# Optimization experiments

Measured on AMD Instinct MI355X. Metric: run time of the kernel, lower is better.

The kernel has to match this reference:

```python
import jax, jax.numpy as jnp
import numpy as np

NUM_HEADS = 16
DIM = 1024


def setup_inputs() -> dict:
    key = jax.random.key(0)
    k1, k2, k3, k4 = jax.random.split(key, 4)
    B, N, C = 4, 2048, DIM
    x = jax.random.normal(k1, (B, N, C), dtype=jnp.float32)
    # weights stored in apply orientation: y = x @ W (+ b)
    W_qkv = jax.random.normal(k2, (C, 3 * C), dtype=jnp.float32) * (C ** -0.5)
    W_out = jax.random.normal(k3, (C, C), dtype=jnp.float32) * (C ** -0.5)
    b_out = jax.random.normal(k4, (C,), dtype=jnp.float32) * 0.01
    return {"hidden_states": x, "W_qkv": W_qkv, "W_out": W_out, "b_out": b_out}


def reference(hidden_states, W_qkv, W_out, b_out):
    B, N, C = hidden_states.shape
    H = NUM_HEADS
    Dh = C // H
    scale = Dh ** -0.5
    qkv = hidden_states @ W_qkv                      # [B, N, 3C]
    qkv = qkv.reshape(B, N, 3, H, Dh).transpose(2, 0, 3, 1, 4)  # [3, B, H, N, Dh]
    q, k, v = qkv[0], qkv[1], qkv[2]
    scores = jnp.einsum('bhnd,bhmd->bhnm', q, k) * scale  # [B, H, N, N]
    probs = jax.nn.softmax(scores, axis=-1)
    out = jnp.einsum('bhnm,bhmd->bhnd', probs, v)    # [B, H, N, Dh]
    out = out.transpose(0, 2, 1, 3).reshape(B, N, C)  # merge heads
    return out @ W_out + b_out                        # dropout p=0 -> identity
```

## Files before the change

### kernel.cpp

```cpp
#include <hip/hip_runtime.h>
#include <hip/hip_bf16.h>
#include <stdint.h>

#define BATCH 4
#define SEQN  2048
#define DIMC  1024
#define NHEADS 16
#define DHEAD 64
#define BH_TOT 64
#define MROWS 8192

typedef __attribute__((ext_vector_type(8))) short bf16x8;
typedef __attribute__((ext_vector_type(4))) float f32x4;

__device__ __forceinline__ unsigned short bf16_rtne(float f){
  union { float f; unsigned u; } v; v.f = f;
  unsigned u = v.u;
  return (unsigned short)((u + 0x7FFFu + ((u >> 16) & 1u)) >> 16);
}
__device__ __forceinline__ float bf16f(unsigned short h){
  union { unsigned u; float f; } v; v.u = ((unsigned)h) << 16;
  return v.f;
}

__device__ __forceinline__ void async16(void* lds, const void* g){
  __builtin_amdgcn_global_load_lds((const __attribute__((address_space(1))) void*)g,
                                   (__attribute__((address_space(3))) void*)lds, 16, 0, 0);
}

__global__ __launch_bounds__(256) void split_rows_k(const float* __restrict__ X,
    unsigned short* __restrict__ O, int nrows, int Kc){
  int q4 = Kc >> 2;
  int total = nrows * q4;
  int idx = blockIdx.x*256 + threadIdx.x;
  if (idx >= total) return;
  int row = idx / q4, c = idx - row*q4;
  const float4 v = *(const float4*)(X + ((size_t)row*Kc + c*4));
  float fv[4] = {v.x, v.y, v.z, v.w};
  unsigned short hi[4], lo[4];
#pragma unroll
  for (int j=0;j<4;j++){ hi[j] = bf16_rtne(fv[j]); lo[j] = bf16_rtne(fv[j] - bf16f(hi[j])); }
  size_t ob = (size_t)row*(2*Kc) + c*4;
  ushort4 h; h.x=hi[0]; h.y=hi[1]; h.z=hi[2]; h.w=hi[3];
  ushort4 l2; l2.x=lo[0]; l2.y=lo[1]; l2.z=lo[2]; l2.w=lo[3];
  *(ushort4*)(O + ob) = h;
  *(ushort4*)(O + ob + Kc) = l2;
}

__global__ __launch_bounds__(256) void transpose_split_k(const float* __restrict__ W,
    unsigned short* __restrict__ Wt, int K, int Nc){
  __shared__ float tile[32][33];
  int tx = threadIdx.x & 31, ty = threadIdx.x >> 5;
  int n0 = blockIdx.x*32, k0 = blockIdx.y*32;
#pragma unroll
  for (int i=0;i<4;i++){
    int k = k0 + ty + i*8;
    tile[ty + i*8][tx] = W[(size_t)k*Nc + n0 + tx];
  }
  __syncthreads();
#pragma unroll
  for (int i=0;i<4;i++){
    int n = n0 + ty + i*8;
    float f = tile[tx][ty + i*8];
    unsigned short hi = bf16_rtne(f);
    unsigned short lo = bf16_rtne(f - bf16f(hi));
    Wt[(size_t)n*(2*K) + k0 + tx] = hi;
    Wt[(size_t)n*(2*K) + K + k0 + tx] = lo;
  }
}

__global__ __launch_bounds__(256) void gemm_split_k(
    const unsigned short* __restrict__ A, const unsigned short* __restrict__ Bt,
    float* __restrict__ C, const float* __restrict__ bias, int M, int Nc, int K)
{
  __shared__ unsigned short a_lds[2][4096];
  __shared__ unsigned short b_lds[2][4096];
  const int t = threadIdx.x, w = t>>6, l = t&63, lg = l>>4, ll = l&15;
  const int wr = w>>1, wc = w&1;
  const int m0 = blockIdx.x*128, n0 = blockIdx.y*128;
  const int ldk = 2*K;
  const int nkt = (3*K) >> 5;
  f32x4 acc[4][4];
#pragma unroll
  for (int m=0;m<4;m++)
#pragma unroll
    for (int n=0;n<4;n++) acc[m][n] = (f32x4){0.f,0.f,0.f,0.f};

  auto stage = [&](int buf, int kt){
    int kp = kt*32;
    int ac = (kp < K)   ? kp : kp - K;
    int bc = (kp < 2*K) ? kp : kp - 2*K;
#pragma unroll
    for (int i=0;i<2;i++){
      int s = t + i*256; int row = s>>2; int sl = s&3; int sl2 = sl ^ (row&3);
      async16(&a_lds[buf][s*8], A + (size_t)(m0+row)*ldk + ac + sl2*8);
    }
#pragma unroll
    for (int i=0;i<2;i++){
      int s = t + i*256; int row = s>>2; int sl = s&3; int sl2 = sl ^ (row&3);
      async16(&b_lds[buf][s*8], Bt + (size_t)(n0+row)*ldk + bc + sl2*8);
    }
  };

  stage(0, 0);
  __syncthreads();
  for (int kt=0; kt<nkt; ++kt){
    int cur = kt&1;
    if (kt+1 < nkt) stage(cur^1, kt+1);
    bf16x8 af[4], bfr[4];
#pragma unroll
    for (int m=0;m<4;m++){
      int row = wr*64 + m*16 + ll;
      af[m] = *(const bf16x8*)&a_lds[cur][row*32 + ((lg ^ (row&3))*8)];
    }
#pragma unroll
    for (int n=0;n<4;n++){
      int row = wc*64 + n*16 + ll;
      bfr[n] = *(const bf16x8*)&b_lds[cur][row*32 + ((lg ^ (row&3))*8)];
    }
#pragma unroll
    for (int m=0;m<4;m++)
#pragma unroll
      for (int n=0;n<4;n++)
        acc[m][n] = __builtin_amdgcn_mfma_f32_16x16x32_bf16(af[m], bfr[n], acc[m][n], 0,0,0);
    __syncthreads();
  }
#pragma unroll
  for (int m=0;m<4;m++)
#pragma unroll
    for (int n=0;n<4;n++){
      int col = n0 + wc*64 + n*16 + ll;
      float bv = bias ? bias[col] : 0.f;
#pragma unroll
      for (int r=0;r<4;r++){
        int row = m0 + wr*64 + m*16 + lg*4 + r;
        C[(size_t)row*Nc + col] = acc[m][n][r] + bv;
      }
    }
}

__global__ __launch_bounds__(256) void split_qk_k(const float* __restrict__ qkv,
    unsigned short* __restrict__ Qo, unsigned short* __restrict__ Ko){
  int idx = blockIdx.x*256 + threadIdx.x;
  int d4 = idx & 15, n = (idx>>4) & (SEQN-1), bh = idx >> 15;
  int b = bh>>4, h = bh&15;
  size_t base = ((size_t)(b*SEQN + n))*3072 + h*64 + d4*4;
  float4 q = *(const float4*)(qkv + base);
  float4 k = *(const float4*)(qkv + base + 1024);
  float fq[4] = {q.x,q.y,q.z,q.w}, fk[4] = {k.x,k.y,k.z,k.w};
  unsigned short qh[4],ql[4],kh[4],kl[4];
#pragma unroll
  for (int j=0;j<4;j++){
    qh[j] = bf16_rtne(fq[j]); ql[j] = bf16_rtne(fq[j] - bf16f(qh[j]));
    kh[j] = bf16_rtne(fk[j]); kl[j] = bf16_rtne(fk[j] - bf16f(kh[j]));
  }
  size_t ob = ((size_t)bh*SEQN + n)*128 + d4*4;
  ushort4 u;
  u.x=qh[0];u.y=qh[1];u.z=qh[2];u.w=qh[3]; *(ushort4*)(Qo+ob) = u;
  u.x=ql[0];u.y=ql[1];u.z=ql[2];u.w=ql[3]; *(ushort4*)(Qo+ob+64) = u;
  u.x=kh[0];u.y=kh[1];u.z=kh[2];u.w=kh[3]; *(ushort4*)(Ko+ob) = u;
  u.x=kl[0];u.y=kl[1];u.z=kl[2];u.w=kl[3]; *(ushort4*)(Ko+ob+64) = u;
}

__global__ __launch_bounds__(256) void build_vt_k(const float* __restrict__ qkv,
    unsigned short* __restrict__ Vt){
  __shared__ float tile[64][65];
  const int mt = blockIdx.x, bh = blockIdx.y;
  const int b = bh>>4, h = bh&15;
  const int t = threadIdx.x;
  const int r = t>>2, seg = t&3;
  size_t src = ((size_t)(b*SEQN + mt*64 + r))*3072 + 2048 + h*64 + seg*16;
#pragma unroll
  for (int j=0;j<4;j++){
    float4 v = *(const float4*)(qkv + src + j*4);
    tile[r][seg*16 + j*4 + 0] = v.x;
    tile[r][seg*16 + j*4 + 1] = v.y;
    tile[r][seg*16 + j*4 + 2] = v.z;
    tile[r][seg*16 + j*4 + 3] = v.w;
  }
  __syncthreads();
  const int d = r, ms = seg;
  unsigned short o16[16];
#pragma unroll
  for (int j=0;j<16;j++) o16[j] = bf16_rtne(tile[ms*16 + j][d]);
  size_t dst = ((size_t)(bh*64 + d))*SEQN + mt*64 + ms*16;
  uint4 u0, u1;
  unsigned* pu = (unsigned*)&u0;
  unsigned* pv = (unsigned*)&u1;
#pragma unroll
  for (int j=0;j<4;j++){
    pu[j] = (unsigned)o16[2*j]   | ((unsigned)o16[2*j+1]<<16);
    pv[j] = (unsigned)o16[8+2*j] | ((unsigned)o16[9+2*j]<<16);
  }
  *(uint4*)(Vt + dst) = u0;
  *(uint4*)(Vt + dst + 8) = u1;
}

__global__ __launch_bounds__(256) void attn_k(const unsigned short* __restrict__ Q,
    const unsigned short* __restrict__ Kh, const unsigned short* __restrict__ Vt,
    float* __restrict__ att)
{
  __shared__ unsigned short k_lds[2][8192];
  __shared__ unsigned short v_lds[2][4096];
  __shared__ unsigned short p_lds[4][1024];
  const int qt = blockIdx.x, bh = blockIdx.y;
  const int b = bh>>4, h = bh&15;
  const int t = threadIdx.x, w = t>>6, l = t&63, lg = l>>4, ll = l&15;
  const size_t kvbase = (size_t)bh*SEQN;

  bf16x8 qf[4];
  {
    size_t qrow = (kvbase + qt*64 + w*16 + ll) * 128;
#pragma unroll
    for (int i=0;i<4;i++)
      qf[i] = *(const bf16x8*)(Q + qrow + i*32 + lg*8);
  }
  f32x4 o[4];
#pragma unroll
  for (int d=0; d<4; d++) o[d] = (f32x4){0.f,0.f,0.f,0.f};
  float lpart[4] = {0.f,0.f,0.f,0.f};

  auto stage = [&](int buf, int kv){
    int m0 = kv*64;
#pragma unroll
    for (int i=0;i<4;i++){
      int s = t + i*256; int row = s>>4; int sl = s&15; int sl2 = sl ^ (row&7);
      async16(&k_lds[buf][s*8], Kh + (kvbase + m0 + row)*128 + sl2*8);
    }
#pragma unroll
    for (int i=0;i<2;i++){
      int s = t + i*256; int row = s>>3; int sl = s&7; int sl2 = sl ^ (row&7);
      async16(&v_lds[buf][s*8], Vt + ((size_t)bh*64 + row)*SEQN + m0 + sl2*8);
    }
  };

  stage(0, 0);
  __syncthreads();
  const int NKV = SEQN/64;
  for (int kv=0; kv<NKV; ++kv){
    int cur = kv&1;
    if (kv+1 < NKV) stage(cur^1, kv+1);
#pragma unroll
    for (int nt=0; nt<4; ++nt){
      bf16x8 kf[4];
      int row = nt*16 + ll;
#pragma unroll
      for (int c=0;c<4;c++){
        int slot = c*4 + lg;
        kf[c] = *(const bf16x8*)&k_lds[cur][row*128 + ((slot ^ (row&7))*8)];
      }
      f32x4 a = (f32x4){0.f,0.f,0.f,0.f};
      a = __builtin_amdgcn_mfma_f32_16x16x32_bf16(qf[0], kf[0], a, 0,0,0);
      a = __builtin_amdgcn_mfma_f32_16x16x32_bf16(qf[1], kf[1], a, 0,0,0);
      a = __builtin_amdgcn_mfma_f32_16x16x32_bf16(qf[0], kf[2], a, 0,0,0);
      a = __builtin_amdgcn_mfma_f32_16x16x32_bf16(qf[1], kf[3], a, 0,0,0);
      a = __builtin_amdgcn_mfma_f32_16x16x32_bf16(qf[2], kf[0], a, 0,0,0);
      a = __builtin_amdgcn_mfma_f32_16x16x32_bf16(qf[3], kf[1], a, 0,0,0);
#pragma unroll
      for (int r=0;r<4;r++){
        float e = __expf(a[r] * 0.125f);
        lpart[r] += e;
        int q = lg*4 + r;
        int col = nt*16 + ll;
        int slot = col >> 3;
        p_lds[w][q*64 + ((slot ^ (q&7))*8) + (col&7)] = bf16_rtne(e);
      }
    }
#pragma unroll
    for (int ks=0; ks<2; ++ks){
      int slot = ks*4 + lg;
      bf16x8 pf = *(const bf16x8*)&p_lds[w][ll*64 + ((slot ^ (ll&7))*8)];
#pragma unroll
      for (int dt=0; dt<4; ++dt){
        int row = dt*16 + ll;
        bf16x8 vf = *(const bf16x8*)&v_lds[cur][row*64 + ((slot ^ (row&7))*8)];
        o[dt] = __builtin_amdgcn_mfma_f32_16x16x32_bf16(pf, vf, o[dt], 0,0,0);
      }
    }
    __syncthreads();
  }
#pragma unroll
  for (int r=0;r<4;r++){
    float s = lpart[r];
    s += __shfl_xor(s, 1);
    s += __shfl_xor(s, 2);
    s += __shfl_xor(s, 4);
    s += __shfl_xor(s, 8);
    float rl = 1.0f / s;
    int qrow = qt*64 + w*16 + lg*4 + r;
    size_t ob = ((size_t)(b*SEQN + qrow))*DIMC + h*64;
#pragma unroll
    for (int dt=0; dt<4; ++dt)
      att[ob + dt*16 + ll] = o[dt][r] * rl;
  }
}

extern "C" void kernel_launch(void* const* d_in, const int* in_sizes, int n_in,
                              void* d_out, int out_size, void* d_ws, size_t ws_size,
                              hipStream_t stream){
  const float* x    = (const float*)d_in[0];
  const float* Wqkv = (const float*)d_in[1];
  const float* Wout = (const float*)d_in[2];
  const float* bout = (const float*)d_in[3];
  float* out = (float*)d_out;

  char* ws = (char*)d_ws;
  size_t off = 0;
  auto walloc = [&](size_t bytes) -> void* {
    void* p = ws + off; off += (bytes + 255) & ~(size_t)255; return p;
  };
  unsigned short* x_hl   = (unsigned short*)walloc((size_t)MROWS*2048*2);
  unsigned short* wqkv_t = (unsigned short*)walloc((size_t)3072*2048*2);
  float*          qkv    = (float*)walloc((size_t)MROWS*3072*4);
  unsigned short* q_hl   = (unsigned short*)walloc((size_t)BH_TOT*SEQN*128*2);
  unsigned short* k_hl   = (unsigned short*)walloc((size_t)BH_TOT*SEQN*128*2);
  unsigned short* vt     = (unsigned short*)walloc((size_t)BH_TOT*64*SEQN*2);
  unsigned short* wout_t = (unsigned short*)walloc((size_t)1024*2048*2);
  float*          att    = qkv;
  unsigned short* att_hl = x_hl;

  split_rows_k<<<8192, 256, 0, stream>>>(x, x_hl, MROWS, DIMC);
  transpose_split_k<<<dim3(3072/32, 1024/32), 256, 0, stream>>>(Wqkv, wqkv_t, 1024, 3072);
  transpose_split_k<<<dim3(1024/32, 1024/32), 256, 0, stream>>>(Wout, wout_t, 1024, 1024);
  gemm_split_k<<<dim3(MROWS/128, 3072/128), 256, 0, stream>>>(x_hl, wqkv_t, qkv, nullptr, MROWS, 3072, 1024);
  split_qk_k<<<(BH_TOT*SEQN*16)/256, 256, 0, stream>>>(qkv, q_hl, k_hl);
  build_vt_k<<<dim3(SEQN/64, BH_TOT), 256, 0, stream>>>(qkv, vt);
  attn_k<<<dim3(SEQN/64, BH_TOT), 256, 0, stream>>>(q_hl, k_hl, vt, att);
  split_rows_k<<<8192, 256, 0, stream>>>(att, att_hl, MROWS, DIMC);
  gemm_split_k<<<dim3(MROWS/128, 1024/128), 256, 0, stream>>>(att_hl, wout_t, out, bout, MROWS, 1024, 1024);
}
```

Measured before the change: 633.6 us.

## Drop K low split, fold softmax scale into Q, remap blocks for L2 locality

Q is pre-scaled by log2(e)/sqrt(Dh) so the attention kernel can use exp2 directly. K keeps only its bf16 high part, which halves K traffic and LDS and cuts the QK MFMAs from six to four. The score tile is computed transposed so each lane packs its P values with v_cvt_pk_bf16 and reduces the row sum with fewer shuffles. Also added: XCD-aware block remapping in both the GEMM and attention kernels, setprio around MFMA groups, and an occupancy hint of 4 on attn_k. Dropping the K low part lowers score precision, and the softmax still has no max subtraction.

```diff
diff --git a/kernel.cpp b/kernel.cpp
--- a/kernel.cpp
+++ b/kernel.cpp
@@ -21,6 +21,11 @@
 __device__ __forceinline__ float bf16f(unsigned short h){
   union { unsigned u; float f; } v; v.u = ((unsigned)h) << 16;
   return v.f;
+}
+__device__ __forceinline__ unsigned cvt_pk_bf16(float lo, float hi){
+  unsigned r;
+  asm("v_cvt_pk_bf16_f32 %0, %1, %2" : "=v"(r) : "v"(lo), "v"(hi));
+  return r;
 }
 
 __device__ __forceinline__ void async16(void* lds, const void* g){
@@ -77,7 +82,11 @@
   __shared__ unsigned short b_lds[2][4096];
   const int t = threadIdx.x, w = t>>6, l = t&63, lg = l>>4, ll = l&15;
   const int wr = w>>1, wc = w&1;
-  const int m0 = blockIdx.x*128, n0 = blockIdx.y*128;
+  const int nbx = gridDim.x;
+  const int nwg = nbx * gridDim.y;
+  const int orig = blockIdx.y*nbx + blockIdx.x;
+  const int id = ((orig & 7) * (nwg >> 3)) + (orig >> 3);
+  const int m0 = (id % nbx)*128, n0 = (id / nbx)*128;
   const int ldk = 2*K;
   const int nkt = (3*K) >> 5;
   f32x4 acc[4][4];
@@ -139,6 +148,7 @@
     }
 }
 
+#define QSCALE 0.18033688f
 __global__ __launch_bounds__(256) void split_qk_k(const float* __restrict__ qkv,
     unsigned short* __restrict__ Qo, unsigned short* __restrict__ Ko){
   int idx = blockIdx.x*256 + threadIdx.x;
@@ -147,19 +157,20 @@
   size_t base = ((size_t)(b*SEQN + n))*3072 + h*64 + d4*4;
   float4 q = *(const float4*)(qkv + base);
   float4 k = *(const float4*)(qkv + base + 1024);
-  float fq[4] = {q.x,q.y,q.z,q.w}, fk[4] = {k.x,k.y,k.z,k.w};
-  unsigned short qh[4],ql[4],kh[4],kl[4];
+  float fq[4] = {q.x*QSCALE, q.y*QSCALE, q.z*QSCALE, q.w*QSCALE};
+  float fk[4] = {k.x, k.y, k.z, k.w};
+  unsigned short qh[4], ql[4], kh[4];
 #pragma unroll
   for (int j=0;j<4;j++){
     qh[j] = bf16_rtne(fq[j]); ql[j] = bf16_rtne(fq[j] - bf16f(qh[j]));
-    kh[j] = bf16_rtne(fk[j]); kl[j] = bf16_rtne(fk[j] - bf16f(kh[j]));
-  }
-  size_t ob = ((size_t)bh*SEQN + n)*128 + d4*4;
+    kh[j] = bf16_rtne(fk[j]);
+  }
+  size_t obq = ((size_t)bh*SEQN + n)*128 + d4*4;
+  size_t obk = ((size_t)bh*SEQN + n)*64 + d4*4;
   ushort4 u;
-  u.x=qh[0];u.y=qh[1];u.z=qh[2];u.w=qh[3]; *(ushort4*)(Qo+ob) = u;
-  u.x=ql[0];u.y=ql[1];u.z=ql[2];u.w=ql[3]; *(ushort4*)(Qo+ob+64) = u;
-  u.x=kh[0];u.y=kh[1];u.z=kh[2];u.w=kh[3]; *(ushort4*)(Ko+ob) = u;
-  u.x=kl[0];u.y=kl[1];u.z=kl[2];u.w=kl[3]; *(ushort4*)(Ko+ob+64) = u;
+  u.x=qh[0];u.y=qh[1];u.z=qh[2];u.w=qh[3]; *(ushort4*)(Qo+obq) = u;
+  u.x=ql[0];u.y=ql[1];u.z=ql[2];u.w=ql[3]; *(ushort4*)(Qo+obq+64) = u;
+  u.x=kh[0];u.y=kh[1];u.z=kh[2];u.w=kh[3]; *(ushort4*)(Ko+obk) = u;
 }
 
 __global__ __launch_bounds__(256) void build_vt_k(const float* __restrict__ qkv,
@@ -196,14 +207,16 @@
   *(uint4*)(Vt + dst + 8) = u1;
 }
 
-__global__ __launch_bounds__(256) void attn_k(const unsigned short* __restrict__ Q,
+__global__ __launch_bounds__(256, 4) void attn_k(const unsigned short* __restrict__ Q,
     const unsigned short* __restrict__ Kh, const unsigned short* __restrict__ Vt,
     float* __restrict__ att)
 {
-  __shared__ unsigned short k_lds[2][8192];
+  __shared__ unsigned short k_lds[2][4096];
   __shared__ unsigned short v_lds[2][4096];
-  __shared__ unsigned short p_lds[4][1024];
-  const int qt = blockIdx.x, bh = blockIdx.y;
+  __shared__ unsigned p_lds[4][512];
+  const int orig = blockIdx.y*gridDim.x + blockIdx.x;
+  const int id = ((orig & 7) << 8) + (orig >> 3);
+  const int qt = id & 31, bh = id >> 5;
   const int b = bh>>4, h = bh&15;
   const int t = threadIdx.x, w = t>>6, l = t&63, lg = l>>4, ll = l&15;
   const size_t kvbase = (size_t)bh*SEQN;
@@ -218,14 +231,14 @@
   f32x4 o[4];
 #pragma unroll
   for (int d=0; d<4; d++) o[d] = (f32x4){0.f,0.f,0.f,0.f};
-  float lpart[4] = {0.f,0.f,0.f,0.f};
+  float lsum = 0.f;
 
   auto stage = [&](int buf, int kv){
     int m0 = kv*64;
 #pragma unroll
-    for (int i=0;i<4;i++){
-      int s = t + i*256; int row = s>>4; int sl = s&15; int sl2 = sl ^ (row&7);
-      async16(&k_lds[buf][s*8], Kh + (kvbase + m0 + row)*128 + sl2*8);
+    for (int i=0;i<2;i++){
+      int s = t + i*256; int row = s>>3; int sl = s&7; int sl2 = sl ^ (row&7);
+      async16(&k_lds[buf][s*8], Kh + (kvbase + m0 + row)*64 + sl2*8);
     }
 #pragma unroll
     for (int i=0;i<2;i++){
@@ -242,51 +255,46 @@
     if (kv+1 < NKV) stage(cur^1, kv+1);
 #pragma unroll
     for (int nt=0; nt<4; ++nt){
-      bf16x8 kf[4];
       int row = nt*16 + ll;
-#pragma unroll
-      for (int c=0;c<4;c++){
-        int slot = c*4 + lg;
-        kf[c] = *(const bf16x8*)&k_lds[cur][row*128 + ((slot ^ (row&7))*8)];
-      }
+      bf16x8 kf0 = *(const bf16x8*)&k_lds[cur][row*64 + (((0*4+lg) ^ (row&7))*8)];
+      bf16x8 kf1 = *(const bf16x8*)&k_lds[cur][row*64 + (((1*4+lg) ^ (row&7))*8)];
       f32x4 a = (f32x4){0.f,0.f,0.f,0.f};
-      a = __builtin_amdgcn_mfma_f32_16x16x32_bf16(qf[0], kf[0], a, 0,0,0);
-      a = __builtin_amdgcn_mfma_f32_16x16x32_bf16(qf[1], kf[1], a, 0,0,0);
-      a = __builtin_amdgcn_mfma_f32_16x16x32_bf16(qf[0], kf[2], a, 0,0,0);
-      a = __builtin_amdgcn_mfma_f32_16x16x32_bf16(qf[1], kf[3], a, 0,0,0);
-      a = __builtin_amdgcn_mfma_f32_16x16x32_bf16(qf[2], kf[0], a, 0,0,0);
-      a = __builtin_amdgcn_mfma_f32_16x16x32_bf16(qf[3], kf[1], a, 0,0,0);
-#pragma unroll
-      for (int r=0;r<4;r++){
-        float e = __expf(a[r] * 0.125f);
-        lpart[r] += e;
-        int q = lg*4 + r;
-        int col = nt*16 + ll;
-        int slot = col >> 3;
-        p_lds[w][q*64 + ((slot ^ (q&7))*8) + (col&7)] = bf16_rtne(e);
-      }
+      __builtin_amdgcn_s_setprio(1);
+      a = __builtin_amdgcn_mfma_f32_16x16x32_bf16(kf0, qf[0], a, 0,0,0);
+      a = __builtin_amdgcn_mfma_f32_16x16x32_bf16(kf1, qf[1], a, 0,0,0);
+      a = __builtin_amdgcn_mfma_f32_16x16x32_bf16(kf0, qf[2], a, 0,0,0);
+      a = __builtin_amdgcn_mfma_f32_16x16x32_bf16(kf1, qf[3], a, 0,0,0);
+      __builtin_amdgcn_s_setprio(0);
+      float e0 = exp2f(a[0]), e1 = exp2f(a[1]), e2 = exp2f(a[2]), e3 = exp2f(a[3]);
+      lsum += (e0 + e1) + (e2 + e3);
+      unsigned pk0 = cvt_pk_bf16(e0, e1);
+      unsigned pk1 = cvt_pk_bf16(e2, e3);
+      int c0 = nt*8 + lg*2;
+      int addr = ll*32 + (((c0>>2) ^ (ll&7))<<2) + (c0&3);
+      *(uint2*)&p_lds[w][addr] = make_uint2(pk0, pk1);
     }
 #pragma unroll
     for (int ks=0; ks<2; ++ks){
-      int slot = ks*4 + lg;
-      bf16x8 pf = *(const bf16x8*)&p_lds[w][ll*64 + ((slot ^ (ll&7))*8)];
+      int chunk = ks*4 + lg;
+      bf16x8 pf = *(const bf16x8*)&p_lds[w][ll*32 + ((chunk ^ (ll&7))<<2)];
+      __builtin_amdgcn_s_setprio(1);
 #pragma unroll
       for (int dt=0; dt<4; ++dt){
         int row = dt*16 + ll;
-        bf16x8 vf = *(const bf16x8*)&v_lds[cur][row*64 + ((slot ^ (row&7))*8)];
+        bf16x8 vf = *(const bf16x8*)&v_lds[cur][row*64 + (((ks*4+lg) ^ (row&7))*8)];
         o[dt] = __builtin_amdgcn_mfma_f32_16x16x32_bf16(pf, vf, o[dt], 0,0,0);
       }
+      __builtin_amdgcn_s_setprio(0);
     }
     __syncthreads();
   }
+  float tot = lsum;
+  tot += __shfl_xor(tot, 16);
+  tot += __shfl_xor(tot, 32);
+  float inv = 1.0f / tot;
 #pragma unroll
   for (int r=0;r<4;r++){
-    float s = lpart[r];
-    s += __shfl_xor(s, 1);
-    s += __shfl_xor(s, 2);
-    s += __shfl_xor(s, 4);
-    s += __shfl_xor(s, 8);
-    float rl = 1.0f / s;
+    float rl = __shfl(inv, lg*4 + r);
     int qrow = qt*64 + w*16 + lg*4 + r;
     size_t ob = ((size_t)(b*SEQN + qrow))*DIMC + h*64;
 #pragma unroll
@@ -313,7 +321,7 @@
   unsigned short* wqkv_t = (unsigned short*)walloc((size_t)3072*2048*2);
   float*          qkv    = (float*)walloc((size_t)MROWS*3072*4);
   unsigned short* q_hl   = (unsigned short*)walloc((size_t)BH_TOT*SEQN*128*2);
-  unsigned short* k_hl   = (unsigned short*)walloc((size_t)BH_TOT*SEQN*128*2);
+  unsigned short* k_h    = (unsigned short*)walloc((size_t)BH_TOT*SEQN*64*2);
   unsigned short* vt     = (unsigned short*)walloc((size_t)BH_TOT*64*SEQN*2);
   unsigned short* wout_t = (unsigned short*)walloc((size_t)1024*2048*2);
   float*          att    = qkv;
@@ -323,9 +331,9 @@
   transpose_split_k<<<dim3(3072/32, 1024/32), 256, 0, stream>>>(Wqkv, wqkv_t, 1024, 3072);
   transpose_split_k<<<dim3(1024/32, 1024/32), 256, 0, stream>>>(Wout, wout_t, 1024, 1024);
   gemm_split_k<<<dim3(MROWS/128, 3072/128), 256, 0, stream>>>(x_hl, wqkv_t, qkv, nullptr, MROWS, 3072, 1024);
-  split_qk_k<<<(BH_TOT*SEQN*16)/256, 256, 0, stream>>>(qkv, q_hl, k_hl);
+  split_qk_k<<<(BH_TOT*SEQN*16)/256, 256, 0, stream>>>(qkv, q_hl, k_h);
   build_vt_k<<<dim3(SEQN/64, BH_TOT), 256, 0, stream>>>(qkv, vt);
-  attn_k<<<dim3(SEQN/64, BH_TOT), 256, 0, stream>>>(q_hl, k_hl, vt, att);
+  attn_k<<<dim3(SEQN/64, BH_TOT), 256, 0, stream>>>(q_hl, k_h, vt, att);
   split_rows_k<<<8192, 256, 0, stream>>>(att, att_hl, MROWS, DIMC);
   gemm_split_k<<<dim3(MROWS/128, 1024/128), 256, 0, stream>>>(att_hl, wout_t, out, bout, MROWS, 1024, 1024);
 }
```

Measured after the change: 545.8 us. -13.9%, faster.
